# Kernel optimization log

Hardware: AMD Instinct MI355X
Metric: run time of the kernel (lower is better)

The kernel has to match this reference:

```python
import jax, jax.numpy as jnp
import numpy as np
from jax import lax

B, T, C_IN, H, K = 8, 4096, 256, 256, 3


def _conv1d_same(x_nct, w_oik, b_o):
    # x: [B, C, T], w: [H, C, K], b: [H] -> [B, H, T], 'same' padding
    y = lax.conv_general_dilated(x_nct, w_oik, window_strides=(1,),
                                 padding='SAME',
                                 dimension_numbers=('NCH', 'OIH', 'NCH'))
    return y + b_o[None, :, None]


def setup_inputs() -> dict:
    key = jax.random.key(0)
    ks = jax.random.split(key, 7)
    std = 1.0 / np.sqrt(H)
    u = lambda k, shape: jax.random.uniform(k, shape, jnp.float32, -std, std)
    return {
        'inputs': jax.random.normal(ks[0], (B, T, C_IN), jnp.float32),
        'init_f': jax.random.normal(ks[1], (B, H), jnp.float32),
        'init_z': jax.random.normal(ks[2], (B, H), jnp.float32),
        'f_w': u(ks[3], (H, C_IN, K)),
        'f_b': u(ks[4], (H,)),
        'z_w': u(ks[5], (H, C_IN, K)),
        'z_b': u(ks[6], (H,)),
    }


def reference(inputs, init_f, init_z, f_w, f_b, z_w, z_b):
    x = jnp.transpose(inputs, (0, 2, 1))                    # [B, C, T]
    raw_f = jnp.transpose(_conv1d_same(x, f_w, f_b), (0, 2, 1))  # [B, T, H]
    raw_z = jnp.transpose(_conv1d_same(x, z_w, z_b), (0, 2, 1))
    # prepend init state along time: init_state[0] -> f, init_state[1] -> z
    raw_f = jnp.concatenate([init_f[:, None, :], raw_f], axis=1)  # [B, T+1, H]
    raw_z = jnp.concatenate([init_z[:, None, :], raw_z], axis=1)
    log_one_minus_f = jax.nn.log_sigmoid(-raw_f)
    log_z = jax.nn.log_sigmoid(raw_z)
    log_f = jax.nn.log_sigmoid(raw_f)
    cs = jnp.cumsum(log_f, axis=1)
    recurrent_gates = log_f - cs + cs[:, -1:, :]
    log_hidden = lax.cumlogsumexp(log_z + log_one_minus_f + recurrent_gates, axis=1)
    return jnp.exp(log_hidden - recurrent_gates)            # [B, T+1, H]
```

## Files before the change

### kernel.cpp

```cpp
#include <hip/hip_runtime.h>
#include <hip/hip_bf16.h>

#define B_ 8
#define T_ 4096
#define C_ 256
#define H_ 256
#define K_ 3
#define NC 128
#define TC 32
#define WFRAG_ELEMS (24 * 32 * 64 * 8)

typedef __attribute__((ext_vector_type(8))) __bf16 bf16x8;
typedef __attribute__((ext_vector_type(4))) float f32x4;

__device__ __forceinline__ float sigm(float x) { return 1.0f / (1.0f + __expf(-x)); }

__device__ __forceinline__ ushort f2bf(float f) {
    union { float f; unsigned u; } v; v.f = f;
    return (ushort)((v.u + 0x7FFFu + ((v.u >> 16) & 1u)) >> 16);
}
__device__ __forceinline__ float bf2f(ushort u) {
    union { unsigned u; float f; } v; v.u = ((unsigned)u) << 16; return v.f;
}

__global__ __launch_bounds__(256) void wfrag_kernel(const float* __restrict__ fw,
                                                    const float* __restrict__ zw,
                                                    ushort* __restrict__ wfrag) {
    int idx = blockIdx.x * 256 + threadIdx.x;
    if (idx >= WFRAG_ELEMS) return;
    int j   = idx & 7;
    int l   = (idx >> 3) & 63;
    int ntg = (idx >> 9) & 31;
    int ks  = idx >> 14;
    int n = ntg * 16 + (l & 15);
    int kappa = ks * 32 + (l >> 4) * 8 + j;
    int k = kappa >> 8, c = kappa & 255;
    const float* w = (n < 256) ? fw : zw;
    int h = n & 255;
    wfrag[idx] = f2bf(w[(h * C_ + c) * K_ + k]);
}

template <int P>
__device__ __forceinline__ void epi_write(f32x4 (&acc)[4][4], unsigned* buf,
                                          int lr, int lg, int h0) {
#pragma unroll
    for (int m2 = 0; m2 < 2; ++m2) {
        const int mi = 2 * P + m2;
#pragma unroll
        for (int ni = 0; ni < 2; ++ni) {
            const int h = h0 + ni * 16 + lr;
#pragma unroll
            for (int r = 0; r < 4; ++r) {
                float fv = sigm(acc[mi][ni][r]);
                float av = sigm(acc[mi][ni + 2][r]) * (1.0f - fv);
                int trow = m2 * 16 + lg * 4 + r;
                buf[trow * 256 + (h ^ ((trow << 2) & 31))] =
                    (unsigned)f2bf(av) | ((unsigned)f2bf(fv) << 16);
            }
        }
    }
}

__global__ __launch_bounds__(512, 4) void conv_scan_kernel(const float* __restrict__ x,
                                                           const ushort* __restrict__ wfrag,
                                                           const float* __restrict__ fb,
                                                           const float* __restrict__ zb,
                                                           unsigned* __restrict__ AP,
                                                           float* __restrict__ fl) {
    __shared__ __align__(16) char smem[66 * 512];
    unsigned* buf = (unsigned*)smem;

    const int b = blockIdx.y;
    const int t0 = blockIdx.x * 64;
    const int tid = threadIdx.x;

    for (int idx = tid; idx < 66 * 64; idx += 512) {
        int row = idx >> 6;
        int c4 = (idx & 63) * 4;
        int t = t0 - 1 + row;
        float4 v = make_float4(0.f, 0.f, 0.f, 0.f);
        if (t >= 0 && t < T_) v = *(const float4*)(x + ((size_t)(b * T_ + t)) * C_ + c4);
        ushort4 w4;
        w4.x = f2bf(v.x); w4.y = f2bf(v.y); w4.z = f2bf(v.z); w4.w = f2bf(v.w);
        *(ushort4*)(smem + row * 512 + ((c4 * 2) ^ ((row & 7) << 4))) = w4;
    }
    __syncthreads();

    const int wv = tid >> 6;
    const int l  = tid & 63;
    const int lr = l & 15;
    const int lg = l >> 4;
    const int h0 = wv * 32;

    f32x4 acc[4][4];
#pragma unroll
    for (int ni = 0; ni < 4; ++ni) {
        float bv = (ni < 2 ? fb : zb)[h0 + (ni & 1) * 16 + lr];
        f32x4 bvv = {bv, bv, bv, bv};
#pragma unroll
        for (int mi = 0; mi < 4; ++mi) acc[mi][ni] = bvv;
    }

    const ushort* wb = wfrag + (size_t)l * 8;

#pragma unroll 1
    for (int ks = 0; ks < 24; ++ks) {
        const int k = ks >> 3;
        const int cb = ((ks & 7) * 32 + lg * 8) * 2;
        bf16x8 afr[4];
#pragma unroll
        for (int mi = 0; mi < 4; ++mi) {
            int row = mi * 16 + lr + k;
            afr[mi] = *(const bf16x8*)(smem + row * 512 + (cb ^ ((row & 7) << 4)));
        }
#pragma unroll
        for (int ni = 0; ni < 4; ++ni) {
            const int ntg = (ni < 2) ? (wv * 2 + ni) : (16 + wv * 2 + ni - 2);
            bf16x8 bfr = *(const bf16x8*)(wb + (size_t)ks * 16384 + (size_t)ntg * 512);
#pragma unroll
            for (int mi = 0; mi < 4; ++mi)
                acc[mi][ni] = __builtin_amdgcn_mfma_f32_16x16x32_bf16(afr[mi], bfr, acc[mi][ni], 0, 0, 0);
        }
    }

    __syncthreads();
    epi_write<0>(acc, buf, lr, lg, h0);
    __syncthreads();
    if (tid < 256) {
        const int h = tid;
        const int chunk = blockIdx.x * 2;
        const int r0 = chunk * TC;
        unsigned* app = AP + ((size_t)b * T_ + r0) * H_ + h;
        unsigned u = buf[0 * 256 + (h ^ 0)];
        float A = bf2f((ushort)(u & 0xffff));
        float P = 1.0f;
        float f_prev = bf2f((ushort)(u >> 16));
        app[0] = (unsigned)f2bf(A) | ((unsigned)f2bf(P) << 16);
#pragma unroll 8
        for (int j = 1; j < TC; ++j) {
            u = buf[j * 256 + (h ^ ((j << 2) & 31))];
            float a = bf2f((ushort)(u & 0xffff));
            float f = bf2f((ushort)(u >> 16));
            A = fmaf(f_prev, A, a);
            P *= f_prev;
            f_prev = f;
            app[(size_t)j * H_] = (unsigned)f2bf(A) | ((unsigned)f2bf(P) << 16);
        }
        fl[((size_t)b * NC + chunk) * H_ + h] = f_prev;
    }

    __syncthreads();
    epi_write<1>(acc, buf, lr, lg, h0);
    __syncthreads();
    if (tid < 256) {
        const int h = tid;
        const int chunk = blockIdx.x * 2 + 1;
        const int r0 = chunk * TC;
        unsigned* app = AP + ((size_t)b * T_ + r0) * H_ + h;
        unsigned u = buf[0 * 256 + (h ^ 0)];
        float A = bf2f((ushort)(u & 0xffff));
        float P = 1.0f;
        float f_prev = bf2f((ushort)(u >> 16));
        app[0] = (unsigned)f2bf(A) | ((unsigned)f2bf(P) << 16);
#pragma unroll 8
        for (int j = 1; j < TC; ++j) {
            u = buf[j * 256 + (h ^ ((j << 2) & 31))];
            float a = bf2f((ushort)(u & 0xffff));
            float f = bf2f((ushort)(u >> 16));
            A = fmaf(f_prev, A, a);
            P *= f_prev;
            f_prev = f;
            app[(size_t)j * H_] = (unsigned)f2bf(A) | ((unsigned)f2bf(P) << 16);
        }
        fl[((size_t)b * NC + chunk) * H_ + h] = f_prev;
    }
}

__global__ __launch_bounds__(256) void combine_kernel(const unsigned* __restrict__ AP,
                                                      const float* __restrict__ fl,
                                                      const float* __restrict__ init_f,
                                                      const float* __restrict__ init_z,
                                                      float* __restrict__ out,
                                                      float* __restrict__ sin_) {
    const int b = blockIdx.x;
    const int h = threadIdx.x;
    float f0 = sigm(init_f[b * H_ + h]);
    float z0 = sigm(init_z[b * H_ + h]);
    float s = z0 * (1.0f - f0);
    out[(size_t)b * (T_ + 1) * H_ + h] = s;
    float flp = f0;
#pragma unroll 4
    for (int c = 0; c < NC; ++c) {
        float st = flp * s;
        sin_[((size_t)b * NC + c) * H_ + h] = st;
        unsigned u = AP[((size_t)b * T_ + c * TC + (TC - 1)) * H_ + h];
        s = fmaf(bf2f((ushort)(u >> 16)), st, bf2f((ushort)(u & 0xffff)));
        flp = fl[((size_t)b * NC + c) * H_ + h];
    }
}

__global__ __launch_bounds__(256) void apply_kernel(const unsigned* __restrict__ AP,
                                                    const float* __restrict__ sin_,
                                                    float* __restrict__ out) {
    const int c = blockIdx.x;
    const int b = blockIdx.y;
    const int h = threadIdx.x;
    const int r0 = c * TC;
    const float s = sin_[((size_t)b * NC + c) * H_ + h];
    const unsigned* app = AP + ((size_t)b * T_ + r0) * H_ + h;
    float* op = out + ((size_t)b * (T_ + 1) + r0 + 1) * H_ + h;
#pragma unroll 8
    for (int j = 0; j < TC; ++j) {
        unsigned u = app[(size_t)j * H_];
        op[(size_t)j * H_] = fmaf(bf2f((ushort)(u >> 16)), s, bf2f((ushort)(u & 0xffff)));
    }
}

extern "C" void kernel_launch(void* const* d_in, const int* in_sizes, int n_in,
                              void* d_out, int out_size, void* d_ws, size_t ws_size,
                              hipStream_t stream) {
    const float* inputs = (const float*)d_in[0];
    const float* init_f = (const float*)d_in[1];
    const float* init_z = (const float*)d_in[2];
    const float* f_w    = (const float*)d_in[3];
    const float* f_b    = (const float*)d_in[4];
    const float* z_w    = (const float*)d_in[5];
    const float* z_b    = (const float*)d_in[6];
    float* out = (float*)d_out;

    ushort* wfrag = (ushort*)d_ws;
    unsigned* AP  = (unsigned*)(wfrag + WFRAG_ELEMS);
    float* fl     = (float*)(AP + (size_t)B_ * T_ * H_);
    float* sin_   = fl + (size_t)B_ * NC * H_;

    wfrag_kernel<<<(WFRAG_ELEMS + 255) / 256, 256, 0, stream>>>(f_w, z_w, wfrag);

    dim3 cgrid(T_ / 64, B_, 1);
    conv_scan_kernel<<<cgrid, 512, 0, stream>>>(inputs, wfrag, f_b, z_b, AP, fl);

    combine_kernel<<<B_, H_, 0, stream>>>(AP, fl, init_f, init_z, out, sin_);

    dim3 agrid(NC, B_, 1);
    apply_kernel<<<agrid, 256, 0, stream>>>(AP, sin_, out);
}
```

Before: 72.06 us.

## Scan both chunks in parallel, compact chunk tails, vectorize apply and hoist LDS addressing

The conv_scan epilogue now writes both 32-row chunks to a larger LDS buffer at once and all 512 threads scan them in parallel, replacing two serialized half-block scans. Each chunk's final (A,P) is also written to a compact APl array, so combine_kernel reads contiguous data with prefetch instead of strided AP rows. apply_kernel switches to float4/uint4 vector loads and stores. The MFMA loop hoists swizzled LDS base addresses per tap. The costs are 64KB of shared memory per block, which may reduce occupancy, and a small extra global buffer.

```diff
diff --git a/kernel.cpp b/kernel.cpp
--- a/kernel.cpp
+++ b/kernel.cpp
@@ -40,34 +40,14 @@
     wfrag[idx] = f2bf(w[(h * C_ + c) * K_ + k]);
 }
 
-template <int P>
-__device__ __forceinline__ void epi_write(f32x4 (&acc)[4][4], unsigned* buf,
-                                          int lr, int lg, int h0) {
-#pragma unroll
-    for (int m2 = 0; m2 < 2; ++m2) {
-        const int mi = 2 * P + m2;
-#pragma unroll
-        for (int ni = 0; ni < 2; ++ni) {
-            const int h = h0 + ni * 16 + lr;
-#pragma unroll
-            for (int r = 0; r < 4; ++r) {
-                float fv = sigm(acc[mi][ni][r]);
-                float av = sigm(acc[mi][ni + 2][r]) * (1.0f - fv);
-                int trow = m2 * 16 + lg * 4 + r;
-                buf[trow * 256 + (h ^ ((trow << 2) & 31))] =
-                    (unsigned)f2bf(av) | ((unsigned)f2bf(fv) << 16);
-            }
-        }
-    }
-}
-
 __global__ __launch_bounds__(512, 4) void conv_scan_kernel(const float* __restrict__ x,
                                                            const ushort* __restrict__ wfrag,
                                                            const float* __restrict__ fb,
                                                            const float* __restrict__ zb,
                                                            unsigned* __restrict__ AP,
+                                                           unsigned* __restrict__ APl,
                                                            float* __restrict__ fl) {
-    __shared__ __align__(16) char smem[66 * 512];
+    __shared__ __align__(16) char smem[65536];
     unsigned* buf = (unsigned*)smem;
 
     const int b = blockIdx.y;
@@ -91,6 +71,7 @@
     const int lr = l & 15;
     const int lg = l >> 4;
     const int h0 = wv * 32;
+    const int lgoff = lg * 16;
 
     f32x4 acc[4][4];
 #pragma unroll
@@ -104,79 +85,81 @@
     const ushort* wb = wfrag + (size_t)l * 8;
 
 #pragma unroll 1
-    for (int ks = 0; ks < 24; ++ks) {
-        const int k = ks >> 3;
-        const int cb = ((ks & 7) * 32 + lg * 8) * 2;
-        bf16x8 afr[4];
+    for (int kg = 0; kg < 3; ++kg) {
+        int abase[4];
 #pragma unroll
         for (int mi = 0; mi < 4; ++mi) {
-            int row = mi * 16 + lr + k;
-            afr[mi] = *(const bf16x8*)(smem + row * 512 + (cb ^ ((row & 7) << 4)));
-        }
-#pragma unroll
-        for (int ni = 0; ni < 4; ++ni) {
-            const int ntg = (ni < 2) ? (wv * 2 + ni) : (16 + wv * 2 + ni - 2);
-            bf16x8 bfr = *(const bf16x8*)(wb + (size_t)ks * 16384 + (size_t)ntg * 512);
+            int row = mi * 16 + lr + kg;
+            int rowx = (row & 7) << 4;
+            abase[mi] = row * 512 + (lgoff ^ (rowx & 48)) + (rowx & 64);
+        }
+#pragma unroll
+        for (int ksp = 0; ksp < 8; ++ksp) {
+            const int ks = kg * 8 + ksp;
+            bf16x8 afr[4];
 #pragma unroll
             for (int mi = 0; mi < 4; ++mi)
-                acc[mi][ni] = __builtin_amdgcn_mfma_f32_16x16x32_bf16(afr[mi], bfr, acc[mi][ni], 0, 0, 0);
+                afr[mi] = *(const bf16x8*)(smem + (abase[mi] ^ (ksp << 6)));
+#pragma unroll
+            for (int ni = 0; ni < 4; ++ni) {
+                const int ntg = (ni < 2) ? (wv * 2 + ni) : (16 + wv * 2 + ni - 2);
+                bf16x8 bfr = *(const bf16x8*)(wb + (size_t)ks * 16384 + (size_t)ntg * 512);
+#pragma unroll
+                for (int mi = 0; mi < 4; ++mi)
+                    acc[mi][ni] = __builtin_amdgcn_mfma_f32_16x16x32_bf16(afr[mi], bfr, acc[mi][ni], 0, 0, 0);
+            }
         }
     }
 
     __syncthreads();
-    epi_write<0>(acc, buf, lr, lg, h0);
+#pragma unroll
+    for (int mi = 0; mi < 4; ++mi) {
+#pragma unroll
+        for (int ni = 0; ni < 2; ++ni) {
+            const int h = h0 + ni * 16 + lr;
+#pragma unroll
+            for (int r = 0; r < 4; ++r) {
+                float fv = sigm(acc[mi][ni][r]);
+                float av = sigm(acc[mi][ni + 2][r]) * (1.0f - fv);
+                int tl = (mi & 1) * 16 + lg * 4 + r;
+                int trow = (mi >> 1) * 32 + tl;
+                buf[trow * 256 + (h ^ ((tl << 2) & 31))] =
+                    (unsigned)f2bf(av) | ((unsigned)f2bf(fv) << 16);
+            }
+        }
+    }
     __syncthreads();
-    if (tid < 256) {
-        const int h = tid;
-        const int chunk = blockIdx.x * 2;
+
+    {
+        const int ch = tid >> 8;
+        const int h = tid & 255;
+        const int chunk = blockIdx.x * 2 + ch;
         const int r0 = chunk * TC;
+        const unsigned* bp = buf + ch * 32 * 256;
         unsigned* app = AP + ((size_t)b * T_ + r0) * H_ + h;
-        unsigned u = buf[0 * 256 + (h ^ 0)];
+        unsigned u = bp[h];
         float A = bf2f((ushort)(u & 0xffff));
         float P = 1.0f;
         float f_prev = bf2f((ushort)(u >> 16));
-        app[0] = (unsigned)f2bf(A) | ((unsigned)f2bf(P) << 16);
+        unsigned upk = (unsigned)f2bf(A) | ((unsigned)f2bf(P) << 16);
+        app[0] = upk;
 #pragma unroll 8
         for (int j = 1; j < TC; ++j) {
-            u = buf[j * 256 + (h ^ ((j << 2) & 31))];
+            u = bp[j * 256 + (h ^ ((j << 2) & 31))];
             float a = bf2f((ushort)(u & 0xffff));
             float f = bf2f((ushort)(u >> 16));
             A = fmaf(f_prev, A, a);
             P *= f_prev;
             f_prev = f;
-            app[(size_t)j * H_] = (unsigned)f2bf(A) | ((unsigned)f2bf(P) << 16);
-        }
+            upk = (unsigned)f2bf(A) | ((unsigned)f2bf(P) << 16);
+            app[(size_t)j * H_] = upk;
+        }
+        APl[((size_t)b * NC + chunk) * H_ + h] = upk;
         fl[((size_t)b * NC + chunk) * H_ + h] = f_prev;
     }
-
-    __syncthreads();
-    epi_write<1>(acc, buf, lr, lg, h0);
-    __syncthreads();
-    if (tid < 256) {
-        const int h = tid;
-        const int chunk = blockIdx.x * 2 + 1;
-        const int r0 = chunk * TC;
-        unsigned* app = AP + ((size_t)b * T_ + r0) * H_ + h;
-        unsigned u = buf[0 * 256 + (h ^ 0)];
-        float A = bf2f((ushort)(u & 0xffff));
-        float P = 1.0f;
-        float f_prev = bf2f((ushort)(u >> 16));
-        app[0] = (unsigned)f2bf(A) | ((unsigned)f2bf(P) << 16);
-#pragma unroll 8
-        for (int j = 1; j < TC; ++j) {
-            u = buf[j * 256 + (h ^ ((j << 2) & 31))];
-            float a = bf2f((ushort)(u & 0xffff));
-            float f = bf2f((ushort)(u >> 16));
-            A = fmaf(f_prev, A, a);
-            P *= f_prev;
-            f_prev = f;
-            app[(size_t)j * H_] = (unsigned)f2bf(A) | ((unsigned)f2bf(P) << 16);
-        }
-        fl[((size_t)b * NC + chunk) * H_ + h] = f_prev;
-    }
-}
-
-__global__ __launch_bounds__(256) void combine_kernel(const unsigned* __restrict__ AP,
+}
+
+__global__ __launch_bounds__(256) void combine_kernel(const unsigned* __restrict__ APl,
                                                       const float* __restrict__ fl,
                                                       const float* __restrict__ init_f,
                                                       const float* __restrict__ init_z,
@@ -189,13 +172,17 @@
     float s = z0 * (1.0f - f0);
     out[(size_t)b * (T_ + 1) * H_ + h] = s;
     float flp = f0;
-#pragma unroll 4
+    const unsigned* ap = APl + (size_t)b * NC * H_ + h;
+    const float* fp = fl + (size_t)b * NC * H_ + h;
+    float* sp = sin_ + (size_t)b * NC * H_ + h;
+#pragma unroll 8
     for (int c = 0; c < NC; ++c) {
+        unsigned u = ap[(size_t)c * H_];
+        float fln = fp[(size_t)c * H_];
         float st = flp * s;
-        sin_[((size_t)b * NC + c) * H_ + h] = st;
-        unsigned u = AP[((size_t)b * T_ + c * TC + (TC - 1)) * H_ + h];
+        sp[(size_t)c * H_] = st;
         s = fmaf(bf2f((ushort)(u >> 16)), st, bf2f((ushort)(u & 0xffff)));
-        flp = fl[((size_t)b * NC + c) * H_ + h];
+        flp = fln;
     }
 }
 
@@ -204,15 +191,21 @@
                                                     float* __restrict__ out) {
     const int c = blockIdx.x;
     const int b = blockIdx.y;
-    const int h = threadIdx.x;
+    const int tid = threadIdx.x;
+    const int jr = tid >> 6;
+    const int h4 = (tid & 63) * 4;
     const int r0 = c * TC;
-    const float s = sin_[((size_t)b * NC + c) * H_ + h];
-    const unsigned* app = AP + ((size_t)b * T_ + r0) * H_ + h;
-    float* op = out + ((size_t)b * (T_ + 1) + r0 + 1) * H_ + h;
-#pragma unroll 8
-    for (int j = 0; j < TC; ++j) {
-        unsigned u = app[(size_t)j * H_];
-        op[(size_t)j * H_] = fmaf(bf2f((ushort)(u >> 16)), s, bf2f((ushort)(u & 0xffff)));
+    const float4 s4 = *(const float4*)(sin_ + ((size_t)b * NC + c) * H_ + h4);
+#pragma unroll
+    for (int p = 0; p < 8; ++p) {
+        const int j = p * 4 + jr;
+        const uint4 u4 = *(const uint4*)(AP + ((size_t)b * T_ + r0 + j) * H_ + h4);
+        float4 o;
+        o.x = fmaf(bf2f((ushort)(u4.x >> 16)), s4.x, bf2f((ushort)(u4.x & 0xffff)));
+        o.y = fmaf(bf2f((ushort)(u4.y >> 16)), s4.y, bf2f((ushort)(u4.y & 0xffff)));
+        o.z = fmaf(bf2f((ushort)(u4.z >> 16)), s4.z, bf2f((ushort)(u4.z & 0xffff)));
+        o.w = fmaf(bf2f((ushort)(u4.w >> 16)), s4.w, bf2f((ushort)(u4.w & 0xffff)));
+        *(float4*)(out + ((size_t)b * (T_ + 1) + r0 + 1 + j) * H_ + h4) = o;
     }
 }
 
@@ -230,15 +223,16 @@
 
     ushort* wfrag = (ushort*)d_ws;
     unsigned* AP  = (unsigned*)(wfrag + WFRAG_ELEMS);
-    float* fl     = (float*)(AP + (size_t)B_ * T_ * H_);
+    unsigned* APl = AP + (size_t)B_ * T_ * H_;
+    float* fl     = (float*)(APl + (size_t)B_ * NC * H_);
     float* sin_   = fl + (size_t)B_ * NC * H_;
 
     wfrag_kernel<<<(WFRAG_ELEMS + 255) / 256, 256, 0, stream>>>(f_w, z_w, wfrag);
 
     dim3 cgrid(T_ / 64, B_, 1);
-    conv_scan_kernel<<<cgrid, 512, 0, stream>>>(inputs, wfrag, f_b, z_b, AP, fl);
-
-    combine_kernel<<<B_, H_, 0, stream>>>(AP, fl, init_f, init_z, out, sin_);
+    conv_scan_kernel<<<cgrid, 512, 0, stream>>>(inputs, wfrag, f_b, z_b, AP, APl, fl);
+
+    combine_kernel<<<B_, H_, 0, stream>>>(APl, fl, init_f, init_z, out, sin_);
 
     dim3 agrid(NC, B_, 1);
     apply_kernel<<<agrid, 256, 0, stream>>>(AP, sin_, out);
```

After: 79.40 us. +10.2%, slower.
